# Kernel optimization log

Measured on AMD Instinct MI355X. Metric: run time of the kernel, lower is better.

The kernel has to match this reference:

```python
import jax, jax.numpy as jnp
import numpy as np

NUM_HEADS = 8
SIGMA = 1.0
LAMBDA_INIT = 0.1
GAMMA_INIT = 0.001


def _pos_encoding(H, W, d_model):
    # 2D sinusoidal encoding: first half encodes x (width), second half y (height)
    d = d_model // 2
    div = jnp.exp(jnp.arange(0, d, 2, dtype=jnp.float32) * (-np.log(10000.0) / d))
    xs = jnp.arange(W, dtype=jnp.float32)[:, None] * div  # (W, d//2)
    ys = jnp.arange(H, dtype=jnp.float32)[:, None] * div  # (H, d//2)
    pe_x = jnp.stack([jnp.sin(xs), jnp.cos(xs)], axis=-1).reshape(W, d)
    pe_y = jnp.stack([jnp.sin(ys), jnp.cos(ys)], axis=-1).reshape(H, d)
    pe = jnp.concatenate([
        jnp.broadcast_to(pe_x[None, :, :], (H, W, d)),
        jnp.broadcast_to(pe_y[:, None, :], (H, W, d)),
    ], axis=-1)
    return pe  # (H, W, d_model)


def _distance_map(H, W, sigma):
    # exp(-euclidean_dist / sigma) between all flattened pixel positions
    yy, xx = jnp.meshgrid(jnp.arange(H, dtype=jnp.float32), jnp.arange(W, dtype=jnp.float32), indexing='ij')
    coords = jnp.stack([yy.reshape(-1), xx.reshape(-1)], axis=-1)  # (HW, 2)
    d2 = jnp.sum((coords[:, None, :] - coords[None, :, :]) ** 2, axis=-1)
    return jnp.exp(-jnp.sqrt(d2) / sigma)  # (HW, HW)


def _conv1x1(x, w, b):
    # 1x1 conv == channel matmul; x: (B,C,H,W), w: (O,C), b: (O,)
    return jnp.einsum('bchw,oc->bohw', x, w) + b[None, :, None, None]


def setup_inputs() -> dict:
    key = jax.random.key(0)
    ks = jax.random.split(key, 9)
    B, C, H, W = 2, 256, 48, 48
    d_model = 256
    inp = {
        'x': jax.random.normal(ks[0], (B, C, H, W), dtype=jnp.float32),
        'Wq': jax.random.normal(ks[1], (d_model, C), dtype=jnp.float32) * 0.01,
        'bq': jnp.zeros((d_model,), dtype=jnp.float32),
        'Wk': jax.random.normal(ks[2], (d_model, C), dtype=jnp.float32) * 0.01,
        'bk': jnp.zeros((d_model,), dtype=jnp.float32),
        'Wv': jax.random.normal(ks[3], (d_model, C), dtype=jnp.float32) * 0.01,
        'bv': jnp.zeros((d_model,), dtype=jnp.float32),
        'Wo': jax.random.normal(ks[4], (C, d_model), dtype=jnp.float32) * 0.01,
        'bo': jnp.zeros((C,), dtype=jnp.float32),
        'lambda_dist': jnp.float32(LAMBDA_INIT),
        'gamma': jnp.float32(GAMMA_INIT),
    }
    return inp


def reference(x, Wq, bq, Wk, bk, Wv, bv, Wo, bo, lambda_dist, gamma):
    B, C, H, W = x.shape
    d_model = Wq.shape[0]
    d_k = d_model // NUM_HEADS
    pe = _pos_encoding(H, W, d_model).transpose(2, 0, 1)[None]  # (1, d_model, H, W)
    dm = _distance_map(H, W, SIGMA)                              # (HW, HW)

    q = _conv1x1(x, Wq, bq) + pe
    k = _conv1x1(x, Wk, bk) + pe
    v = _conv1x1(x, Wv, bv)

    def heads(t):
        return t.reshape(B, NUM_HEADS, d_k, H * W).transpose(0, 1, 3, 2)  # (B,h,HW,d_k)

    Q, K, V = heads(q), heads(k), heads(v)
    scores = jnp.einsum('bhnd,bhmd->bhnm', Q, K) / jnp.sqrt(jnp.float32(d_k))
    scores = scores + (lambda_dist * dm)[None, None]  # 'exp' distance prior bias
    attn = jax.nn.softmax(scores, axis=-1)
    out = jnp.einsum('bhnm,bhmd->bhnd', attn, V)
    out = out.transpose(0, 1, 3, 2).reshape(B, d_model, H, W)
    fused = gamma * out  # simple weighted fusion, single (self) branch
    return x + _conv1x1(fused, Wo, bo)
```

## Files before the change

### kernel.cpp

```cpp
#include <hip/hip_runtime.h>

#define HW 2304
#define SW 48
#define DMODEL 256
#define NHEADS 8
#define DK 32
#define BATCH 2

typedef unsigned short u16;
typedef __attribute__((ext_vector_type(8))) short short8;
typedef __attribute__((ext_vector_type(4))) float f32x4;

__device__ __forceinline__ float bf2f(u16 v) {
  union { unsigned int u; float f; } c; c.u = ((unsigned int)v) << 16; return c.f;
}
__device__ __forceinline__ float lo2f(unsigned int u) {
  union { unsigned int u; float f; } c; c.u = u << 16; return c.f;
}
__device__ __forceinline__ float hi2f(unsigned int u) {
  union { unsigned int u; float f; } c; c.u = u & 0xffff0000u; return c.f;
}
__device__ __forceinline__ u16 f2bf(float f) {
  union { unsigned int u; float f; } c; c.f = f;
  unsigned int u = c.u;
  unsigned int r = (u + 0x7FFFu + ((u >> 16) & 1u)) >> 16;
  return (u16)r;
}
__device__ __forceinline__ unsigned int pkbf(float a, float b) {
  union { float f; unsigned int u; } ca, cb;
  ca.f = a; cb.f = b;
  return __builtin_amdgcn_perm(ca.u, cb.u, 0x03020706u);
}
__device__ __forceinline__ int div48(int n) { return (n * 87382) >> 22; }
__device__ __forceinline__ int swz(int row, int k) {
  return ((row >> 4) << 12) + ((k >> 3) << 7) + ((row & 15) << 3) + (k & 7);
}

__global__ __launch_bounds__(256) void prep_kernel(
    const float* __restrict__ x,
    const float* __restrict__ Wq, const float* __restrict__ Wk,
    const float* __restrict__ Wv, const float* __restrict__ Wo,
    const float* __restrict__ lam_p,
    u16* __restrict__ xt, u16* __restrict__ Wb, u16* __restrict__ et) {
  int bid = blockIdx.x;
  int t = threadIdx.x;
  if (bid < 288) {
    int b = bid / 144, r = bid % 144;
    int c0 = (r / 36) * 64, n0 = (r % 36) * 64;
    __shared__ u16 sh[64][72];
#pragma unroll
    for (int p = 0; p < 4; ++p) {
      int row = (t >> 4) + p * 16;
      int col4 = (t & 15) * 4;
      float4 v = *(const float4*)(x + (size_t)(b * DMODEL + c0 + row) * HW +
                                  n0 + col4);
      sh[col4 + 0][row] = f2bf(v.x);
      sh[col4 + 1][row] = f2bf(v.y);
      sh[col4 + 2][row] = f2bf(v.z);
      sh[col4 + 3][row] = f2bf(v.w);
    }
    __syncthreads();
    u16* xtb = xt + (size_t)b * HW * DMODEL;
#pragma unroll
    for (int q = 0; q < 2; ++q) {
      int nrow = t >> 2;
      int c8 = (t & 3) * 8 + q * 32;
      *(uint4*)(xtb + swz(n0 + nrow, c0 + c8)) = *(const uint4*)&sh[nrow][c8];
    }
  } else if (bid < 544) {
    int idx = (bid - 288) * 1024 + t * 4;
    int which = idx >> 16, off = idx & 65535;
    int m = off >> 8, k = off & 255;
    const float* src = (which == 0) ? Wq : (which == 1) ? Wk
                       : (which == 2) ? Wv : Wo;
    float4 v = *(const float4*)(src + off);
    ushort4 ov;
    ov.x = f2bf(v.x); ov.y = f2bf(v.y); ov.z = f2bf(v.z); ov.w = f2bf(v.w);
    *(ushort4*)(Wb + which * 65536 + swz(m, k)) = ov;
  } else {
    int id = (bid - 544) * 256 + t;
    int flat = id * 8;
    int tile = flat >> 8;
    int within = flat & 255;
    int tm = tile / 144, tq = tile - tm * 144;
    int m = tm * 16 + (within >> 4);
    int q = tq * 16 + (within & 15);
    int ym = div48(m), xm = m - ym * SW;
    int yq = div48(q), xq = q - yq * SW;
    float lam = lam_p[0];
    float dy = (float)(yq - ym);
    float dy2 = dy * dy;
    u16 o[8];
#pragma unroll
    for (int j = 0; j < 8; ++j) {
      float dx = (float)(xq + j - xm);
      o[j] = f2bf(lam * __expf(-sqrtf(dy2 + dx * dx)));
    }
    *(uint4*)(et + flat) = *(const uint4*)o;
  }
}

__global__ __launch_bounds__(256) void qkv_kernel(
    const u16* __restrict__ Wb, const u16* __restrict__ xt,
    const float* __restrict__ bq, const float* __restrict__ bk,
    const float* __restrict__ bv,
    u16* __restrict__ qt, u16* __restrict__ ktb, u16* __restrict__ vb) {
  int t = threadIdx.x;
  int w = t >> 6, lane = t & 63, lo = lane & 15, quad = lane >> 4;
  int n0 = blockIdx.x * 64;
  int mb = blockIdx.y, b = blockIdx.z;
  int which = mb >> 2;
  int mrel0 = (mb & 3) * 64;
  const u16* A = Wb + which * 65536 + ((mrel0 + w * 16) >> 4) * 4096 + lo * 8;
  const float* bias = (which == 0) ? bq : (which == 1) ? bk : bv;
  const u16* Bx = xt + (size_t)b * HW * DMODEL + lo * 8;

  f32x4 acc[4] = {{0.f, 0.f, 0.f, 0.f}, {0.f, 0.f, 0.f, 0.f},
                  {0.f, 0.f, 0.f, 0.f}, {0.f, 0.f, 0.f, 0.f}};
#pragma unroll
  for (int k0 = 0; k0 < DMODEL; k0 += 32) {
    int kblk = ((k0 >> 3) + quad) << 7;
    short8 af = *(const short8*)(A + kblk);
#pragma unroll
    for (int nt = 0; nt < 4; ++nt) {
      short8 bf_ = *(const short8*)(Bx + ((n0 + nt * 16) >> 4) * 4096 + kblk);
      acc[nt] = __builtin_amdgcn_mfma_f32_16x16x32_bf16(af, bf_, acc[nt], 0, 0, 0);
    }
  }

  int mbase = mrel0 + w * 16 + quad * 4;
  if (which == 2) {
#pragma unroll
    for (int reg = 0; reg < 4; ++reg) {
      int mrel = mbase + reg;
      float bi = bias[mrel];
      u16* dst = vb + (size_t)(b * DMODEL + mrel) * HW + n0 + lo;
#pragma unroll
      for (int nt = 0; nt < 4; ++nt) dst[nt * 16] = f2bf(acc[nt][reg] + bi);
    }
  } else {
    float sc = (which == 0) ? 0.17677669529663687f : 1.0f;
    int h = mbase >> 5, d0 = mbase & 31;
    u16* base = ((which == 0) ? qt : ktb) + (size_t)(b * NHEADS + h) * HW * DK;
    float bi[4], dv[4];
    bool usecos[4], usey[4];
#pragma unroll
    for (int reg = 0; reg < 4; ++reg) {
      int mrel = mbase + reg;
      bi[reg] = bias[mrel];
      int oo = mrel & 127;
      dv[reg] = expf(-0.07195578415606394f * (float)(oo & ~1));
      usecos[reg] = (oo & 1);
      usey[reg] = (mrel >= 128);
    }
#pragma unroll
    for (int nt = 0; nt < 4; ++nt) {
      int n = n0 + nt * 16 + lo;
      int yy = div48(n), xx = n - yy * SW;
      ushort4 ov;
      float vals[4];
#pragma unroll
      for (int reg = 0; reg < 4; ++reg) {
        float tv = (usey[reg] ? (float)yy : (float)xx) * dv[reg];
        float pe = usecos[reg] ? cosf(tv) : sinf(tv);
        vals[reg] = (acc[nt][reg] + bi[reg] + pe) * sc;
      }
      ov.x = f2bf(vals[0]); ov.y = f2bf(vals[1]);
      ov.z = f2bf(vals[2]); ov.w = f2bf(vals[3]);
      *(ushort4*)(base + (size_t)n * DK + d0) = ov;
    }
  }
}

__global__ __launch_bounds__(256) void attn_kernel(
    const u16* __restrict__ qt, const u16* __restrict__ ktb,
    const u16* __restrict__ vb, const u16* __restrict__ et,
    u16* __restrict__ po_o, float* __restrict__ po_l) {
  int t = threadIdx.x;
  int w = t >> 6;
  int lane = t & 63;
  int lo = lane & 15, quad = lane >> 4;
  int n0 = blockIdx.x * 64;
  int h = blockIdx.y >> 2, kh = blockIdx.y & 3;
  int b = blockIdx.z;

  __shared__ u16 Ks[2][64 * 40];
  __shared__ u16 Vs[2][32 * 72];

  const u16* qtg = qt + (size_t)(b * NHEADS + h) * HW * DK;
  const u16* ktg = ktb + (size_t)(b * NHEADS + h) * HW * DK;
  const u16* vbg = vb + (size_t)(b * DMODEL + h * DK) * HW;

  short8 qf = *(const short8*)(qtg + (size_t)(n0 + w * 16 + lo) * DK + quad * 8);

  int srow = t >> 2;
  int sks = srow >> 5, srr = srow & 31;
  int sv = (srr < 16) ? (8 * (srr >> 2) + (srr & 3))
                      : (8 * ((srr - 16) >> 2) + 4 + ((srr - 16) & 3));
  int skey = sks * 32 + sv;
  int sc8 = (t & 3) * 8;
  int vdd = t >> 3, vmo = (t & 7) * 8;

  int tq = (n0 >> 4) + w;
  const u16* etw = et + (size_t)tq * 144 * 256 + lo * 16 + (quad & 1) * 8;
  int qh = quad >> 1;

  f32x4 o0 = {0.f, 0.f, 0.f, 0.f}, o1 = {0.f, 0.f, 0.f, 0.f};
  float lsum = 0.f;

  const int kt0 = kh * 9;
  {
    int m0 = kt0 * 64;
    *(uint4*)&Ks[0][srow * 40 + sc8] =
        *(const uint4*)(ktg + (size_t)(m0 + skey) * DK + sc8);
    *(uint4*)&Vs[0][vdd * 72 + vmo] =
        *(const uint4*)(vbg + (size_t)vdd * HW + m0 + vmo);
  }
  __syncthreads();

  for (int i = 0; i < 9; ++i) {
    int cur = i & 1;
    if (i + 1 < 9) {
      int m1 = (kt0 + i + 1) * 64;
      *(uint4*)&Ks[cur ^ 1][srow * 40 + sc8] =
          *(const uint4*)(ktg + (size_t)(m1 + skey) * DK + sc8);
      *(uint4*)&Vs[cur ^ 1][vdd * 72 + vmo] =
          *(const uint4*)(vbg + (size_t)vdd * HW + m1 + vmo);
    }

    int m0 = (kt0 + i) * 64;
    uint4 eb0 = *(const uint4*)(etw + (size_t)((m0 >> 4) + 0 + qh) * 256);
    uint4 eb1 = *(const uint4*)(etw + (size_t)((m0 >> 4) + 2 + qh) * 256);

#pragma unroll
    for (int ks = 0; ks < 2; ++ks) {
      uint4 ebv = ks ? eb1 : eb0;
      short8 kfA = *(const short8*)&Ks[cur][(ks * 32 + lo) * 40 + quad * 8];
      short8 kfB = *(const short8*)&Ks[cur][(ks * 32 + 16 + lo) * 40 + quad * 8];
      f32x4 z = {0.f, 0.f, 0.f, 0.f};
      f32x4 sA = __builtin_amdgcn_mfma_f32_16x16x32_bf16(kfA, qf, z, 0, 0, 0);
      f32x4 sB = __builtin_amdgcn_mfma_f32_16x16x32_bf16(kfB, qf, z, 0, 0, 0);
      float p0 = __expf(sA[0] + lo2f(ebv.x));
      float p1 = __expf(sA[1] + hi2f(ebv.x));
      float p2 = __expf(sA[2] + lo2f(ebv.y));
      float p3 = __expf(sA[3] + hi2f(ebv.y));
      float p4 = __expf(sB[0] + lo2f(ebv.z));
      float p5 = __expf(sB[1] + hi2f(ebv.z));
      float p6 = __expf(sB[2] + lo2f(ebv.w));
      float p7 = __expf(sB[3] + hi2f(ebv.w));
      lsum += ((p0 + p1) + (p2 + p3)) + ((p4 + p5) + (p6 + p7));
      unsigned int pk32[4] = {pkbf(p0, p1), pkbf(p2, p3),
                              pkbf(p4, p5), pkbf(p6, p7)};
      short8 pfrag = *(const short8*)pk32;
      short8 v0 = *(const short8*)&Vs[cur][lo * 72 + ks * 32 + quad * 8];
      o0 = __builtin_amdgcn_mfma_f32_16x16x32_bf16(v0, pfrag, o0, 0, 0, 0);
      short8 v1 = *(const short8*)&Vs[cur][(16 + lo) * 72 + ks * 32 + quad * 8];
      o1 = __builtin_amdgcn_mfma_f32_16x16x32_bf16(v1, pfrag, o1, 0, 0, 0);
    }
    __syncthreads();
  }

  lsum += __shfl_xor(lsum, 16);
  lsum += __shfl_xor(lsum, 32);

  int slot = (b * NHEADS + h) * 36 + blockIdx.x;
  u16* pw = po_o + (size_t)(kh * 576 + slot) * 2048 + w * 512;
  uint2 s0, s1;
  s0.x = pkbf(o0[0], o0[1]); s0.y = pkbf(o0[2], o0[3]);
  s1.x = pkbf(o1[0], o1[1]); s1.y = pkbf(o1[2], o1[3]);
  *(uint2*)(pw + lane * 4) = s0;
  *(uint2*)(pw + 256 + lane * 4) = s1;
  if (quad == 0)
    po_l[(size_t)(kh * 576 + slot) * 64 + w * 16 + lo] = lsum;
}

__global__ __launch_bounds__(256) void reduce_kernel(
    const u16* __restrict__ po_o, const float* __restrict__ po_l,
    u16* __restrict__ aot) {
  int t = threadIdx.x;
  int w = t >> 6, lane = t & 63, lo = lane & 15, quad = lane >> 4;
  int qt_ = blockIdx.x, h = blockIdx.y, b = blockIdx.z;
  int slot = (b * NHEADS + h) * 36 + qt_;

  float s0[4] = {0.f, 0.f, 0.f, 0.f}, s1[4] = {0.f, 0.f, 0.f, 0.f};
  float lt = 0.f;
#pragma unroll
  for (int kh = 0; kh < 4; ++kh) {
    const u16* p = po_o + (size_t)(kh * 576 + slot) * 2048 + w * 512;
    ushort4 a0 = *(const ushort4*)(p + lane * 4);
    ushort4 a1 = *(const ushort4*)(p + 256 + lane * 4);
    s0[0] += bf2f(a0.x); s0[1] += bf2f(a0.y);
    s0[2] += bf2f(a0.z); s0[3] += bf2f(a0.w);
    s1[0] += bf2f(a1.x); s1[1] += bf2f(a1.y);
    s1[2] += bf2f(a1.z); s1[3] += bf2f(a1.w);
    lt += po_l[(size_t)(kh * 576 + slot) * 64 + w * 16 + lo];
  }
  float inv = 1.0f / lt;

  int n = qt_ * 64 + w * 16 + lo;
  u16* aog = aot + (size_t)b * HW * DMODEL;
  ushort4 w0, w1;
  w0.x = f2bf(s0[0] * inv); w0.y = f2bf(s0[1] * inv);
  w0.z = f2bf(s0[2] * inv); w0.w = f2bf(s0[3] * inv);
  w1.x = f2bf(s1[0] * inv); w1.y = f2bf(s1[1] * inv);
  w1.z = f2bf(s1[2] * inv); w1.w = f2bf(s1[3] * inv);
  *(ushort4*)&aog[swz(n, h * DK + quad * 4)] = w0;
  *(ushort4*)&aog[swz(n, h * DK + 16 + quad * 4)] = w1;
}

__global__ __launch_bounds__(256) void out_kernel(
    const float* __restrict__ x, const u16* __restrict__ Wob,
    const float* __restrict__ bo, const float* __restrict__ gp,
    const u16* __restrict__ aot, float* __restrict__ out) {
  int t = threadIdx.x;
  int w = t >> 6, lane = t & 63, lo = lane & 15, quad = lane >> 4;
  int n0 = blockIdx.x * 64;
  int c0 = blockIdx.y * 64;
  int b = blockIdx.z;
  float gamma = gp[0];
  const u16* A = Wob + ((c0 + w * 16) >> 4) * 4096 + lo * 8;
  const u16* Ba = aot + (size_t)b * HW * DMODEL + lo * 8;

  f32x4 acc[4] = {{0.f, 0.f, 0.f, 0.f}, {0.f, 0.f, 0.f, 0.f},
                  {0.f, 0.f, 0.f, 0.f}, {0.f, 0.f, 0.f, 0.f}};
#pragma unroll
  for (int k0 = 0; k0 < DMODEL; k0 += 32) {
    int kblk = ((k0 >> 3) + quad) << 7;
    short8 af = *(const short8*)(A + kblk);
#pragma unroll
    for (int nt = 0; nt < 4; ++nt) {
      short8 bf_ = *(const short8*)(Ba + ((n0 + nt * 16) >> 4) * 4096 + kblk);
      acc[nt] = __builtin_amdgcn_mfma_f32_16x16x32_bf16(af, bf_, acc[nt], 0, 0, 0);
    }
  }

#pragma unroll
  for (int reg = 0; reg < 4; ++reg) {
    int c = c0 + w * 16 + quad * 4 + reg;
    float bi = bo[c];
    const float* xs = x + (size_t)(b * DMODEL + c) * HW + n0 + lo;
    float* os = out + (size_t)(b * DMODEL + c) * HW + n0 + lo;
#pragma unroll
    for (int nt = 0; nt < 4; ++nt)
      os[nt * 16] = xs[nt * 16] + gamma * acc[nt][reg] + bi;
  }
}

extern "C" void kernel_launch(void* const* d_in, const int* in_sizes, int n_in,
                              void* d_out, int out_size, void* d_ws,
                              size_t ws_size, hipStream_t stream) {
  const float* x   = (const float*)d_in[0];
  const float* Wq  = (const float*)d_in[1];
  const float* bq  = (const float*)d_in[2];
  const float* Wk  = (const float*)d_in[3];
  const float* bk  = (const float*)d_in[4];
  const float* Wv  = (const float*)d_in[5];
  const float* bv  = (const float*)d_in[6];
  const float* Wo  = (const float*)d_in[7];
  const float* bo  = (const float*)d_in[8];
  const float* lam = (const float*)d_in[9];
  const float* gam = (const float*)d_in[10];

  char* wsb = (char*)d_ws;
  u16* Wb  = (u16*)(wsb + 36864);
  u16* xt  = (u16*)(wsb + 561152);
  u16* aot = xt;
  u16* qt  = (u16*)(wsb + 2920448);
  u16* ktb = (u16*)(wsb + 5279744);
  u16* vb  = (u16*)(wsb + 7639040);
  u16* et  = (u16*)(wsb + 9998336);
  u16* po_o = (u16*)(wsb + 20615168);
  float* po_l = (float*)(wsb + 30052352);
  float* out = (float*)d_out;

  prep_kernel<<<dim3(3136), 256, 0, stream>>>(x, Wq, Wk, Wv, Wo, lam,
                                              xt, Wb, et);
  qkv_kernel<<<dim3(36, 12, BATCH), 256, 0, stream>>>(Wb, xt, bq, bk, bv,
                                                      qt, ktb, vb);
  attn_kernel<<<dim3(36, 32, BATCH), 256, 0, stream>>>(qt, ktb, vb, et,
                                                       po_o, po_l);
  reduce_kernel<<<dim3(36, 8, BATCH), 256, 0, stream>>>(po_o, po_l, aot);
  out_kernel<<<dim3(36, 4, BATCH), 256, 0, stream>>>(x, Wb + 3 * 65536, bo, gam,
                                                     aot, out);
}
```

Baseline: 129.1 us.

## Fuse split-KV partial reduction into output projection kernel

Removes the separate reduce kernel. The attention kernel now writes its partial outputs directly in the swizzled layout the output GEMM reads, and the out kernel sums the four key-split partials and applies the softmax normalization while building its B fragments. This saves one launch and one write-then-read of the intermediate. In exchange, each out block (four per batch/position tile) re-reads all four partials, so the partial reads are repeated across channel tiles.

Result: slower. 143.6 us (+11.3%).

```diff
diff --git a/kernel.cpp b/kernel.cpp
--- a/kernel.cpp
+++ b/kernel.cpp
@@ -6,6 +6,7 @@
 #define NHEADS 8
 #define DK 32
 #define BATCH 2
+#define POSTRIDE (BATCH * HW * DMODEL)
 
 typedef unsigned short u16;
 typedef __attribute__((ext_vector_type(8))) short short8;
@@ -263,63 +264,42 @@
   lsum += __shfl_xor(lsum, 16);
   lsum += __shfl_xor(lsum, 32);
 
-  int slot = (b * NHEADS + h) * 36 + blockIdx.x;
-  u16* pw = po_o + (size_t)(kh * 576 + slot) * 2048 + w * 512;
+  int n = n0 + w * 16 + lo;
+  u16* pw = po_o + (size_t)kh * POSTRIDE + (size_t)b * HW * DMODEL;
   uint2 s0, s1;
   s0.x = pkbf(o0[0], o0[1]); s0.y = pkbf(o0[2], o0[3]);
   s1.x = pkbf(o1[0], o1[1]); s1.y = pkbf(o1[2], o1[3]);
-  *(uint2*)(pw + lane * 4) = s0;
-  *(uint2*)(pw + 256 + lane * 4) = s1;
+  *(uint2*)(pw + swz(n, h * DK + quad * 4)) = s0;
+  *(uint2*)(pw + swz(n, h * DK + 16 + quad * 4)) = s1;
   if (quad == 0)
-    po_l[(size_t)(kh * 576 + slot) * 64 + w * 16 + lo] = lsum;
-}
-
-__global__ __launch_bounds__(256) void reduce_kernel(
-    const u16* __restrict__ po_o, const float* __restrict__ po_l,
-    u16* __restrict__ aot) {
-  int t = threadIdx.x;
-  int w = t >> 6, lane = t & 63, lo = lane & 15, quad = lane >> 4;
-  int qt_ = blockIdx.x, h = blockIdx.y, b = blockIdx.z;
-  int slot = (b * NHEADS + h) * 36 + qt_;
-
-  float s0[4] = {0.f, 0.f, 0.f, 0.f}, s1[4] = {0.f, 0.f, 0.f, 0.f};
-  float lt = 0.f;
-#pragma unroll
-  for (int kh = 0; kh < 4; ++kh) {
-    const u16* p = po_o + (size_t)(kh * 576 + slot) * 2048 + w * 512;
-    ushort4 a0 = *(const ushort4*)(p + lane * 4);
-    ushort4 a1 = *(const ushort4*)(p + 256 + lane * 4);
-    s0[0] += bf2f(a0.x); s0[1] += bf2f(a0.y);
-    s0[2] += bf2f(a0.z); s0[3] += bf2f(a0.w);
-    s1[0] += bf2f(a1.x); s1[1] += bf2f(a1.y);
-    s1[2] += bf2f(a1.z); s1[3] += bf2f(a1.w);
-    lt += po_l[(size_t)(kh * 576 + slot) * 64 + w * 16 + lo];
-  }
-  float inv = 1.0f / lt;
-
-  int n = qt_ * 64 + w * 16 + lo;
-  u16* aog = aot + (size_t)b * HW * DMODEL;
-  ushort4 w0, w1;
-  w0.x = f2bf(s0[0] * inv); w0.y = f2bf(s0[1] * inv);
-  w0.z = f2bf(s0[2] * inv); w0.w = f2bf(s0[3] * inv);
-  w1.x = f2bf(s1[0] * inv); w1.y = f2bf(s1[1] * inv);
-  w1.z = f2bf(s1[2] * inv); w1.w = f2bf(s1[3] * inv);
-  *(ushort4*)&aog[swz(n, h * DK + quad * 4)] = w0;
-  *(ushort4*)&aog[swz(n, h * DK + 16 + quad * 4)] = w1;
+    po_l[((size_t)(kh * BATCH + b) * NHEADS + h) * HW + n] = lsum;
 }
 
 __global__ __launch_bounds__(256) void out_kernel(
     const float* __restrict__ x, const u16* __restrict__ Wob,
     const float* __restrict__ bo, const float* __restrict__ gp,
-    const u16* __restrict__ aot, float* __restrict__ out) {
+    const u16* __restrict__ po_o, const float* __restrict__ po_l,
+    float* __restrict__ out) {
   int t = threadIdx.x;
   int w = t >> 6, lane = t & 63, lo = lane & 15, quad = lane >> 4;
   int n0 = blockIdx.x * 64;
   int c0 = blockIdx.y * 64;
   int b = blockIdx.z;
   float gamma = gp[0];
+
+  __shared__ float linv[NHEADS * 64];
+  for (int idx = t; idx < NHEADS * 64; idx += 256) {
+    int h = idx >> 6, nn = idx & 63;
+    float s = 0.f;
+#pragma unroll
+    for (int kh = 0; kh < 4; ++kh)
+      s += po_l[((size_t)(kh * BATCH + b) * NHEADS + h) * HW + n0 + nn];
+    linv[idx] = 1.0f / s;
+  }
+  __syncthreads();
+
   const u16* A = Wob + ((c0 + w * 16) >> 4) * 4096 + lo * 8;
-  const u16* Ba = aot + (size_t)b * HW * DMODEL + lo * 8;
+  const u16* Bp = po_o + (size_t)b * HW * DMODEL + lo * 8;
 
   f32x4 acc[4] = {{0.f, 0.f, 0.f, 0.f}, {0.f, 0.f, 0.f, 0.f},
                   {0.f, 0.f, 0.f, 0.f}, {0.f, 0.f, 0.f, 0.f}};
@@ -327,9 +307,26 @@
   for (int k0 = 0; k0 < DMODEL; k0 += 32) {
     int kblk = ((k0 >> 3) + quad) << 7;
     short8 af = *(const short8*)(A + kblk);
+    int h = k0 >> 5;
 #pragma unroll
     for (int nt = 0; nt < 4; ++nt) {
-      short8 bf_ = *(const short8*)(Ba + ((n0 + nt * 16) >> 4) * 4096 + kblk);
+      size_t boff = (size_t)((n0 + nt * 16) >> 4) * 4096 + kblk;
+      uint4 q0 = *(const uint4*)(Bp + 0 * POSTRIDE + boff);
+      uint4 q1 = *(const uint4*)(Bp + 1 * POSTRIDE + boff);
+      uint4 q2 = *(const uint4*)(Bp + 2 * POSTRIDE + boff);
+      uint4 q3 = *(const uint4*)(Bp + 3 * POSTRIDE + boff);
+      float inv = linv[h * 64 + nt * 16 + lo];
+      float f0 = (lo2f(q0.x) + lo2f(q1.x) + lo2f(q2.x) + lo2f(q3.x)) * inv;
+      float f1 = (hi2f(q0.x) + hi2f(q1.x) + hi2f(q2.x) + hi2f(q3.x)) * inv;
+      float f2 = (lo2f(q0.y) + lo2f(q1.y) + lo2f(q2.y) + lo2f(q3.y)) * inv;
+      float f3 = (hi2f(q0.y) + hi2f(q1.y) + hi2f(q2.y) + hi2f(q3.y)) * inv;
+      float f4 = (lo2f(q0.z) + lo2f(q1.z) + lo2f(q2.z) + lo2f(q3.z)) * inv;
+      float f5 = (hi2f(q0.z) + hi2f(q1.z) + hi2f(q2.z) + hi2f(q3.z)) * inv;
+      float f6 = (lo2f(q0.w) + lo2f(q1.w) + lo2f(q2.w) + lo2f(q3.w)) * inv;
+      float f7 = (hi2f(q0.w) + hi2f(q1.w) + hi2f(q2.w) + hi2f(q3.w)) * inv;
+      unsigned int pk32[4] = {pkbf(f0, f1), pkbf(f2, f3),
+                              pkbf(f4, f5), pkbf(f6, f7)};
+      short8 bf_ = *(const short8*)pk32;
       acc[nt] = __builtin_amdgcn_mfma_f32_16x16x32_bf16(af, bf_, acc[nt], 0, 0, 0);
     }
   }
@@ -364,7 +361,6 @@
   char* wsb = (char*)d_ws;
   u16* Wb  = (u16*)(wsb + 36864);
   u16* xt  = (u16*)(wsb + 561152);
-  u16* aot = xt;
   u16* qt  = (u16*)(wsb + 2920448);
   u16* ktb = (u16*)(wsb + 5279744);
   u16* vb  = (u16*)(wsb + 7639040);
@@ -379,7 +375,6 @@
                                                       qt, ktb, vb);
   attn_kernel<<<dim3(36, 32, BATCH), 256, 0, stream>>>(qt, ktb, vb, et,
                                                        po_o, po_l);
-  reduce_kernel<<<dim3(36, 8, BATCH), 256, 0, stream>>>(po_o, po_l, aot);
   out_kernel<<<dim3(36, 4, BATCH), 256, 0, stream>>>(x, Wb + 3 * 65536, bo, gam,
-                                                     aot, out);
-}
+                                                     po_o, po_l, out);
+}
```
